# Optimization experiments

Measured on AMD Instinct MI355X. Metric: run time of the kernel, lower is better.

## Reference

```python
import math
import jax, jax.numpy as jnp
import numpy as np

B, LA, LB, H = 16, 1024, 1024, 512
NEG = -10000000.0


def setup_inputs() -> dict:
    key = jax.random.key(0)
    k1, k2, k3, k4 = jax.random.split(key, 4)
    a = jax.random.normal(k1, (B, LA, H), dtype=jnp.float32)
    b = jax.random.normal(k2, (B, LB, H), dtype=jnp.float32)
    mask_a = jax.random.randint(k3, (B, LA, 1), 0, 2, dtype=jnp.int32)
    mask_b = jax.random.randint(k4, (B, LB, 1), 0, 2, dtype=jnp.int32)
    temperature = jnp.asarray(1.0 / math.sqrt(H), dtype=jnp.float32)
    return {"a": a, "b": b, "mask_a": mask_a, "mask_b": mask_b, "temperature": temperature}


def reference(a, b, mask_a, mask_b, temperature):
    # attn[b,i,j] = <a_i, b_j> * temperature  -> [B, LA, LB]
    attn = jnp.einsum("bid,bjd->bij", a, b) * temperature
    # pairwise validity mask: outer product of per-token masks
    mask = jnp.einsum("bik,bjk->bij", mask_a.astype(jnp.float32), mask_b.astype(jnp.float32)) > 0
    attn = jnp.where(mask, attn, NEG)
    attn_a = jax.nn.softmax(attn, axis=1)  # softmax over a-tokens
    attn_b = jax.nn.softmax(attn, axis=2)  # softmax over b-tokens
    feature_b = jnp.einsum("bij,bid->bjd", attn_a, a)  # [B, LB, H]
    feature_a = jnp.einsum("bij,bjd->bid", attn_b, b)  # [B, LA, H]
    return (feature_a, feature_b)
```

## Files before the change

### kernel.cpp

```cpp
#include <hip/hip_runtime.h>
#include <hip/hip_bf16.h>

#define NB_ 16
#define LA_ 1024
#define LB_ 1024
#define H_  512

typedef __attribute__((ext_vector_type(8))) short short8;
typedef __attribute__((ext_vector_type(4))) float f32x4;

using bf16 = __hip_bfloat16;

__device__ __forceinline__ float bf2f(unsigned short u) {
    union { unsigned int i; float f; } c; c.i = ((unsigned)u) << 16; return c.f;
}
__device__ __forceinline__ unsigned short f2bf(float f) {
    bf16 h = __float2bfloat16(f);
    return *(unsigned short*)&h;
}

__device__ __forceinline__ void load_lds16(const void* g, void* l) {
    __builtin_amdgcn_global_load_lds(
        (const __attribute__((address_space(1))) void*)g,
        (__attribute__((address_space(3))) void*)l, 16, 0, 0);
}

template<int DB, int MODE>
__device__ __forceinline__ void gemm_tile_cnt(
    const unsigned short* __restrict__ gA, const unsigned short* __restrict__ gB,
    int lda, int ldb, size_t ko,
    unsigned short* lds, char* lA, char* lB,
    const int* aoff, const int* boff, f32x4 acc[8][4])
{
    const char* bA = (const char*)lds + DB * 32768;
    const char* bB = (const char*)lds + 65536 + DB * 32768;
    const int nxt = (DB ^ 1) * 32768;
    short8 av[4][2];
#pragma unroll
    for (int p = 0; p < 4; ++p) {
        const int pm = p >> 1, pn = p & 1;
        if (pn == 0) {
#pragma unroll
            for (int f = 0; f < 4; f++)
#pragma unroll
                for (int kk = 0; kk < 2; kk++)
                    av[f][kk] = *(const short8*)(bA + (aoff[pm * 4 + f] ^ (kk << 6)));
        }
        short8 bv[2][2];
#pragma unroll
        for (int f = 0; f < 2; f++)
#pragma unroll
            for (int kk = 0; kk < 2; kk++)
                bv[f][kk] = *(const short8*)(bB + (boff[pn * 2 + f] ^ (kk << 6)));
        if (MODE == 0) {
            if (p == 0) {
                load_lds16(gB + ko,                       lB + nxt);
                load_lds16(gB + ko + (size_t)64 * ldb,    lB + nxt + 8192);
            } else if (p == 1) {
                load_lds16(gB + ko + (size_t)128 * ldb,   lB + nxt + 16384);
                load_lds16(gB + ko + (size_t)192 * ldb,   lB + nxt + 24576);
            } else if (p == 2) {
                load_lds16(gA + ko,                       lA + nxt);
                load_lds16(gA + ko + (size_t)128 * lda,   lA + nxt + 16384);
            } else {
                load_lds16(gA + ko + (size_t)64 * lda,    lA + nxt + 8192);
                load_lds16(gA + ko + (size_t)192 * lda,   lA + nxt + 24576);
            }
        }
        __builtin_amdgcn_s_barrier();
        __builtin_amdgcn_s_setprio(1);
#pragma unroll
        for (int kk = 0; kk < 2; kk++)
#pragma unroll
            for (int f = 0; f < 2; f++)
#pragma unroll
                for (int m = 0; m < 4; m++)
                    acc[pm * 4 + m][pn * 2 + f] =
                        __builtin_amdgcn_mfma_f32_16x16x32_bf16(
                            av[m][kk], bv[f][kk],
                            acc[pm * 4 + m][pn * 2 + f], 0, 0, 0);
        __builtin_amdgcn_s_setprio(0);
        if (p == 1) {
            if (MODE == 0) asm volatile("s_waitcnt vmcnt(4)" ::: "memory");
            else           asm volatile("s_waitcnt vmcnt(0)" ::: "memory");
        }
        if (p == 3 && MODE == 0) asm volatile("s_waitcnt vmcnt(2)" ::: "memory");
        if (p < 3 || MODE == 0) __builtin_amdgcn_s_barrier();
    }
}

template<int DB, int MODE>
__device__ __forceinline__ void gemm_tile_drn(
    const unsigned short* __restrict__ gA, const unsigned short* __restrict__ gB,
    int lda, int ldb, size_t ko,
    unsigned short* lds, char* lA, char* lB,
    const int* aoff, const int* boff, f32x4 acc[8][4])
{
    const char* bA = (const char*)lds + DB * 32768;
    const char* bB = (const char*)lds + 65536 + DB * 32768;
    const int nxt = (DB ^ 1) * 32768;
    if (MODE == 0) {
#pragma unroll
        for (int s = 0; s < 4; s++) {
            load_lds16(gA + ko + (size_t)(s * 64) * lda, lA + nxt + s * 8192);
            load_lds16(gB + ko + (size_t)(s * 64) * ldb, lB + nxt + s * 8192);
        }
    }
    short8 av[4][2];
#pragma unroll
    for (int p = 0; p < 4; ++p) {
        const int pm = p >> 1, pn = p & 1;
        if (pn == 0) {
#pragma unroll
            for (int f = 0; f < 4; f++)
#pragma unroll
                for (int kk = 0; kk < 2; kk++)
                    av[f][kk] = *(const short8*)(bA + (aoff[pm * 4 + f] ^ (kk << 6)));
        }
        short8 bv[2][2];
#pragma unroll
        for (int f = 0; f < 2; f++)
#pragma unroll
            for (int kk = 0; kk < 2; kk++)
                bv[f][kk] = *(const short8*)(bB + (boff[pn * 2 + f] ^ (kk << 6)));
        __builtin_amdgcn_s_barrier();
        __builtin_amdgcn_s_setprio(1);
#pragma unroll
        for (int kk = 0; kk < 2; kk++)
#pragma unroll
            for (int f = 0; f < 2; f++)
#pragma unroll
                for (int m = 0; m < 4; m++)
                    acc[pm * 4 + m][pn * 2 + f] =
                        __builtin_amdgcn_mfma_f32_16x16x32_bf16(
                            av[m][kk], bv[f][kk],
                            acc[pm * 4 + m][pn * 2 + f], 0, 0, 0);
        __builtin_amdgcn_s_setprio(0);
        if (p < 3) __builtin_amdgcn_s_barrier();
    }
    __syncthreads();
}

template<int SCHED>
__device__ __forceinline__ void gemm_core256(
    const unsigned short* __restrict__ A, const unsigned short* __restrict__ B,
    int lda, int ldb, int K,
    unsigned short* lds, f32x4 acc[8][4])
{
    const int t = threadIdx.x;
    const int w = t >> 6, lane = t & 63;
    const int wr = w >> 2, wc = w & 3;
    const int lm = lane & 15, q = lane >> 4;

    int aoff[8], boff[4];
#pragma unroll
    for (int f = 0; f < 8; f++) {
        const int ra = wr * 128 + f * 16 + lm;
        aoff[f] = ra * 128 + ((q ^ (ra & 7)) << 4);
    }
#pragma unroll
    for (int f = 0; f < 4; f++) {
        const int rb = wc * 64 + f * 16 + lm;
        boff[f] = rb * 128 + ((q ^ (rb & 7)) << 4);
    }

    const int rstep = w * 8 + (lane >> 3);
    const int sc = (lane & 7) ^ (lane >> 3);
    const unsigned short* gA = A + (size_t)rstep * lda + sc * 8;
    const unsigned short* gB = B + (size_t)rstep * ldb + sc * 8;
    char* lA = (char*)lds + w * 1024;
    char* lB = (char*)lds + 65536 + w * 1024;
    const int NT = K >> 6;

    if (SCHED == 0) {
        load_lds16(gB,                       lB);
        load_lds16(gB + (size_t)64 * ldb,    lB + 8192);
        load_lds16(gB + (size_t)128 * ldb,   lB + 16384);
        load_lds16(gB + (size_t)192 * ldb,   lB + 24576);
        load_lds16(gA,                       lA);
        load_lds16(gA + (size_t)128 * lda,   lA + 16384);
        load_lds16(gA + (size_t)64 * lda,    lA + 8192);
        load_lds16(gA + (size_t)192 * lda,   lA + 24576);
        asm volatile("s_waitcnt vmcnt(2)" ::: "memory");
        __builtin_amdgcn_s_barrier();
        int kt = 0;
        for (; kt + 2 < NT; kt += 2) {
            gemm_tile_cnt<0, 0>(gA, gB, lda, ldb, (size_t)(kt + 1) * 64,
                                lds, lA, lB, aoff, boff, acc);
            gemm_tile_cnt<1, 0>(gA, gB, lda, ldb, (size_t)(kt + 2) * 64,
                                lds, lA, lB, aoff, boff, acc);
        }
        gemm_tile_cnt<0, 0>(gA, gB, lda, ldb, (size_t)(NT - 1) * 64,
                            lds, lA, lB, aoff, boff, acc);
        gemm_tile_cnt<1, 1>(gA, gB, lda, ldb, 0, lds, lA, lB, aoff, boff, acc);
    } else {
#pragma unroll
        for (int s = 0; s < 4; s++) {
            load_lds16(gA + (size_t)(s * 64) * lda, lA + s * 8192);
            load_lds16(gB + (size_t)(s * 64) * ldb, lB + s * 8192);
        }
        __syncthreads();
        int kt = 0;
        for (; kt + 2 < NT; kt += 2) {
            gemm_tile_drn<0, 0>(gA, gB, lda, ldb, (size_t)(kt + 1) * 64,
                                lds, lA, lB, aoff, boff, acc);
            gemm_tile_drn<1, 0>(gA, gB, lda, ldb, (size_t)(kt + 2) * 64,
                                lds, lA, lB, aoff, boff, acc);
        }
        gemm_tile_drn<0, 0>(gA, gB, lda, ldb, (size_t)(NT - 1) * 64,
                            lds, lA, lB, aoff, boff, acc);
        gemm_tile_drn<1, 1>(gA, gB, lda, ldb, 0, lds, lA, lB, aoff, boff, acc);
    }
    __syncthreads();
}

__global__ __launch_bounds__(512, 2) void k_gemm_attn(
    const unsigned short* __restrict__ a_bf, const unsigned short* __restrict__ b_bf,
    const int* __restrict__ mask_a, const int* __restrict__ mask_b,
    const float* __restrict__ temp_p,
    unsigned short* __restrict__ E, unsigned short* __restrict__ ET,
    float* __restrict__ l_row, float* __restrict__ l_col)
{
    __shared__ unsigned short lds[65536];

    const int g = blockIdx.x;
    const int batch = g & 15;
    const int qq = g >> 4;
    const int i0 = (qq >> 2) * 256, j0 = (qq & 3) * 256;

    const unsigned short* A = a_bf + (size_t)batch * LA_ * H_ + (size_t)i0 * H_;
    const unsigned short* B = b_bf + (size_t)batch * LB_ * H_ + (size_t)j0 * H_;
    f32x4 acc[8][4];
#pragma unroll
    for (int x = 0; x < 8; x++)
#pragma unroll
        for (int y = 0; y < 4; y++) acc[x][y] = 0;

    gemm_core256<1>(A, B, H_, H_, H_, lds, acc);

    const float temp = temp_p[0];
    const int t = threadIdx.x, w = t >> 6, lane = t & 63;
    const int wr = w >> 2, wc = w & 3, lm = lane & 15, q = lane >> 4;
    const int* map = mask_a + batch * LA_;
    const int* mbp = mask_b + batch * LB_;
    unsigned short* Ep  = E  + (size_t)batch * LA_ * LB_;
    unsigned short* ETp = ET + (size_t)batch * LB_ * LA_;
    float* lrp = l_row + batch * LA_;
    float* lcp = l_col + batch * LB_;

    int mb4[4];
#pragma unroll
    for (int fn = 0; fn < 4; fn++) mb4[fn] = mbp[j0 + wc * 64 + fn * 16 + lm];

#pragma unroll
    for (int fm = 0; fm < 8; fm++) {
        const int ilb = wr * 128 + fm * 16 + q * 4;
        int ma[4];
#pragma unroll
        for (int r = 0; r < 4; r++) ma[r] = map[i0 + ilb + r];
#pragma unroll
        for (int fn = 0; fn < 4; fn++) {
            const int jl = wc * 64 + fn * 16 + lm;
            ushort4 pk;
            unsigned short* pp = (unsigned short*)&pk;
#pragma unroll
            for (int r = 0; r < 4; r++) {
                const float e = (ma[r] && mb4[fn]) ? __expf(acc[fm][fn][r] * temp) : 0.0f;
                acc[fm][fn][r] = e;
                pp[r] = f2bf(e);
                const int il = ilb + r;
                lds[il * 256 + ((((jl >> 3) ^ ((il >> 1) & 15)) << 3) | (jl & 7))] = pp[r];
            }
            *(ushort4*)(ETp + (size_t)(j0 + jl) * LA_ + i0 + ilb) = pk;
        }
    }

#pragma unroll
    for (int fm = 0; fm < 8; fm++)
#pragma unroll
        for (int r = 0; r < 4; r++) {
            float s = acc[fm][0][r] + acc[fm][1][r] + acc[fm][2][r] + acc[fm][3][r];
            s += __shfl_xor(s, 1, 16); s += __shfl_xor(s, 2, 16);
            s += __shfl_xor(s, 4, 16); s += __shfl_xor(s, 8, 16);
            if (lm == 0) atomicAdd(&lrp[i0 + wr * 128 + fm * 16 + q * 4 + r], s);
        }
#pragma unroll
    for (int fn = 0; fn < 4; fn++) {
        float s = 0.0f;
#pragma unroll
        for (int fm = 0; fm < 8; fm++)
#pragma unroll
            for (int r = 0; r < 4; r++) s += acc[fm][fn][r];
        s += __shfl_xor(s, 16, 64); s += __shfl_xor(s, 32, 64);
        if (lane < 16) atomicAdd(&lcp[j0 + wc * 64 + fn * 16 + lm], s);
    }

    __syncthreads();
#pragma unroll
    for (int rep = 0; rep < 16; rep++) {
        const int il = (t >> 5) + rep * 16;
        const int c = t & 31;
        const int phys = c ^ ((il >> 1) & 15);
        short8 v = *(const short8*)(lds + il * 256 + phys * 8);
        *(short8*)(Ep + (size_t)(i0 + il) * LB_ + j0 + c * 8) = v;
    }
}

__global__ __launch_bounds__(512, 2) void k_gemm_feat(
    const unsigned short* __restrict__ E, const unsigned short* __restrict__ ET,
    const unsigned short* __restrict__ aT, const unsigned short* __restrict__ bT,
    const int* __restrict__ mask_a, const int* __restrict__ mask_b,
    const int* __restrict__ nA, const int* __restrict__ nB,
    const float* __restrict__ l_row, const float* __restrict__ l_col,
    const float* __restrict__ mean_a, const float* __restrict__ mean_b,
    float* __restrict__ out)
{
    __shared__ unsigned short lds[65536];

    const int g = blockIdx.x;
    const int zc = g & 31;
    const int qq = g >> 5;
    const int n0 = (qq & 1) * 256, m0 = (qq >> 1) * 256;

    const int batch = zc & 15;
    const bool isA = zc < 16;
    const unsigned short* Amat = (isA ? E : ET) + (size_t)batch * 1024 * 1024;
    const unsigned short* Bm   = (isA ? bT : aT) + (size_t)batch * H_ * 1024;
    const int* mp   = (isA ? mask_a : mask_b) + batch * 1024;
    const int nn    = (isA ? nB : nA)[batch];
    const float* sp = (isA ? l_row : l_col) + batch * 1024;
    const float* mv = (isA ? mean_b : mean_a) + batch * H_;
    float* op = out + (isA ? (size_t)0 : (size_t)NB_ * LA_ * H_) + (size_t)batch * 1024 * H_;

    f32x4 acc[8][4];
#pragma unroll
    for (int x = 0; x < 8; x++)
#pragma unroll
        for (int y = 0; y < 4; y++) acc[x][y] = 0;

    gemm_core256<0>(Amat + (size_t)m0 * 1024, Bm + (size_t)n0 * 1024,
                    1024, 1024, 1024, lds, acc);

    const int t = threadIdx.x, w = t >> 6, lane = t & 63;
    const int wr = w >> 2, wc = w & 3, lm = lane & 15, q = lane >> 4;

    float mval[4];
#pragma unroll
    for (int fn = 0; fn < 4; fn++) mval[fn] = mv[n0 + wc * 64 + fn * 16 + lm];

#pragma unroll
    for (int fm = 0; fm < 8; fm++) {
        const int ib = m0 + wr * 128 + fm * 16 + q * 4;
#pragma unroll
        for (int r = 0; r < 4; r++) {
            const int i = ib + r;
            const bool valid = (mp[i] != 0) && (nn > 0);
            const float inv = valid ? 1.0f / sp[i] : 0.0f;
#pragma unroll
            for (int fn = 0; fn < 4; fn++) {
                const int d = n0 + wc * 64 + fn * 16 + lm;
                op[(size_t)i * H_ + d] = valid ? acc[fm][fn][r] * inv : mval[fn];
            }
        }
    }
}

__global__ __launch_bounds__(256) void k_prep(
    const float* __restrict__ a, const float* __restrict__ b,
    unsigned short* __restrict__ aN, unsigned short* __restrict__ bN,
    unsigned short* __restrict__ aT, unsigned short* __restrict__ bT,
    float* __restrict__ mean_a, float* __restrict__ mean_b,
    const int* __restrict__ mask_a, const int* __restrict__ mask_b,
    int* __restrict__ nA, int* __restrict__ nB,
    float* __restrict__ zero_base)
{
    const int g = blockIdx.x, t = threadIdx.x;
    if (g >= 256) {
        const int s = g - 256;
        *(float4*)(zero_base + ((size_t)s * 256 + t) * 4) = make_float4(0, 0, 0, 0);
        const int batch = s & 15, which = s >> 4;
        const int* m = (which ? mask_b : mask_a) + batch * 1024;
        int cnt = m[t] + m[t + 256] + m[t + 512] + m[t + 768];
        __shared__ int red[256];
        red[t] = cnt;
        __syncthreads();
        for (int off = 128; off; off >>= 1) {
            if (t < off) red[t] += red[t + off];
            __syncthreads();
        }
        if (t == 0) (which ? nB : nA)[batch] = red[0];
        return;
    }
    const int dstrip = g & 7, batch = (g >> 3) & 15, sel = g >> 7;
    const float* src = (sel ? b : a) + (size_t)batch * 1024 * H_;
    unsigned short* np = (sel ? bN : aN) + (size_t)batch * 1024 * H_;
    unsigned short* tp = (sel ? bT : aT) + (size_t)batch * H_ * 1024;
    float* mdst = (sel ? mean_b : mean_a) + batch * H_;
    const int d0 = dstrip * 64;

    __shared__ unsigned short lds[64][68];
    __shared__ float cs[4][64];
    const int c4 = (t & 15) * 4;
    float colsum[4] = {0.f, 0.f, 0.f, 0.f};
    for (int i0 = 0; i0 < 1024; i0 += 64) {
#pragma unroll
        for (int it = 0; it < 4; it++) {
            const int r = (t >> 4) + it * 16;
            float4 v = *(const float4*)(src + (size_t)(i0 + r) * H_ + d0 + c4);
            colsum[0] += v.x; colsum[1] += v.y; colsum[2] += v.z; colsum[3] += v.w;
            ushort4 u = make_ushort4(f2bf(v.x), f2bf(v.y), f2bf(v.z), f2bf(v.w));
            *(ushort4*)(np + (size_t)(i0 + r) * H_ + d0 + c4) = u;
            *(ushort4*)&lds[r][c4] = u;
        }
        __syncthreads();
#pragma unroll
        for (int it = 0; it < 4; it++) {
            const int dd = (t >> 4) + it * 16;
            const int i4 = (t & 15) * 4;
            ushort4 u = make_ushort4(lds[i4][dd], lds[i4 + 1][dd],
                                     lds[i4 + 2][dd], lds[i4 + 3][dd]);
            *(ushort4*)(tp + (size_t)(d0 + dd) * 1024 + i0 + i4) = u;
        }
        __syncthreads();
    }
#pragma unroll
    for (int j = 0; j < 4; j++) {
        colsum[j] += __shfl_xor(colsum[j], 16, 64);
        colsum[j] += __shfl_xor(colsum[j], 32, 64);
    }
    const int w = t >> 6, lane = t & 63;
    if (lane < 16) {
#pragma unroll
        for (int j = 0; j < 4; j++) cs[w][c4 + j] = colsum[j];
    }
    __syncthreads();
    if (t < 64) mdst[d0 + t] = (cs[0][t] + cs[1][t] + cs[2][t] + cs[3][t]) * (1.0f / 1024.0f);
}

extern "C" void kernel_launch(void* const* d_in, const int* in_sizes, int n_in,
                              void* d_out, int out_size, void* d_ws, size_t ws_size,
                              hipStream_t stream)
{
    const float* a      = (const float*)d_in[0];
    const float* b      = (const float*)d_in[1];
    const int*   mask_a = (const int*)d_in[2];
    const int*   mask_b = (const int*)d_in[3];
    const float* temp   = (const float*)d_in[4];
    float* out = (float*)d_out;

    char* ws = (char*)d_ws;
    size_t off = 0;
    unsigned short* E    = (unsigned short*)(ws + off); off += (size_t)NB_ * LA_ * LB_ * 2;
    unsigned short* ET   = (unsigned short*)(ws + off); off += (size_t)NB_ * LB_ * LA_ * 2;
    unsigned short* a_bf = (unsigned short*)(ws + off); off += (size_t)NB_ * LA_ * H_ * 2;
    unsigned short* b_bf = (unsigned short*)(ws + off); off += (size_t)NB_ * LB_ * H_ * 2;
    unsigned short* aT   = (unsigned short*)(ws + off); off += (size_t)NB_ * H_ * LA_ * 2;
    unsigned short* bT   = (unsigned short*)(ws + off); off += (size_t)NB_ * H_ * LB_ * 2;
    float* l_row  = (float*)(ws + off); off += (size_t)NB_ * LA_ * 4;
    float* l_col  = (float*)(ws + off); off += (size_t)NB_ * LB_ * 4;
    float* mean_a = (float*)(ws + off); off += (size_t)NB_ * H_ * 4;
    float* mean_b = (float*)(ws + off); off += (size_t)NB_ * H_ * 4;
    int*   nA     = (int*)(ws + off); off += 64;
    int*   nB     = (int*)(ws + off); off += 64;

    k_prep<<<dim3(288), 256, 0, stream>>>(
        a, b, a_bf, b_bf, aT, bT, mean_a, mean_b,
        mask_a, mask_b, nA, nB, l_row);

    k_gemm_attn<<<dim3(256), 512, 0, stream>>>(
        a_bf, b_bf, mask_a, mask_b, temp, E, ET, l_row, l_col);

    k_gemm_feat<<<dim3(256), 512, 0, stream>>>(
        E, ET, aT, bT, mask_a, mask_b, nA, nB, l_row, l_col, mean_a, mean_b, out);
}
```

Baseline: 203.1 us.

## Fuse prep and both GEMM kernels into one cooperative kernel with grid syncs

Merges the prep, attention-GEMM and feature-GEMM kernels into a single cooperative launch of 256 blocks of 512 threads, separated by grid-wide barriers. The prep stage is re-tiled to 512 threads per block, and the mask-count and l_row zeroing are folded into a subset of blocks. The aim is to remove the inter-kernel launch gaps and tail drain between the three stages. In exchange it adds grid.sync overhead and requires all 256 blocks to be co-resident, and the prep stage now runs on fewer, larger blocks than before (256 blocks of 512 threads instead of 288 blocks of 256).

```diff
diff --git a/kernel.cpp b/kernel.cpp
--- a/kernel.cpp
+++ b/kernel.cpp
@@ -1,5 +1,8 @@
 #include <hip/hip_runtime.h>
 #include <hip/hip_bf16.h>
+#include <hip/hip_cooperative_groups.h>
+
+namespace cg = cooperative_groups;
 
 #define NB_ 16
 #define LA_ 1024
@@ -214,227 +217,229 @@
     __syncthreads();
 }
 
-__global__ __launch_bounds__(512, 2) void k_gemm_attn(
-    const unsigned short* __restrict__ a_bf, const unsigned short* __restrict__ b_bf,
+__global__ __launch_bounds__(512, 2) void k_fused(
+    const float* __restrict__ a, const float* __restrict__ b,
     const int* __restrict__ mask_a, const int* __restrict__ mask_b,
     const float* __restrict__ temp_p,
+    unsigned short* __restrict__ a_bf, unsigned short* __restrict__ b_bf,
+    unsigned short* __restrict__ aT, unsigned short* __restrict__ bT,
     unsigned short* __restrict__ E, unsigned short* __restrict__ ET,
-    float* __restrict__ l_row, float* __restrict__ l_col)
-{
-    __shared__ unsigned short lds[65536];
-
-    const int g = blockIdx.x;
-    const int batch = g & 15;
-    const int qq = g >> 4;
-    const int i0 = (qq >> 2) * 256, j0 = (qq & 3) * 256;
-
-    const unsigned short* A = a_bf + (size_t)batch * LA_ * H_ + (size_t)i0 * H_;
-    const unsigned short* B = b_bf + (size_t)batch * LB_ * H_ + (size_t)j0 * H_;
-    f32x4 acc[8][4];
-#pragma unroll
-    for (int x = 0; x < 8; x++)
-#pragma unroll
-        for (int y = 0; y < 4; y++) acc[x][y] = 0;
-
-    gemm_core256<1>(A, B, H_, H_, H_, lds, acc);
-
-    const float temp = temp_p[0];
-    const int t = threadIdx.x, w = t >> 6, lane = t & 63;
-    const int wr = w >> 2, wc = w & 3, lm = lane & 15, q = lane >> 4;
-    const int* map = mask_a + batch * LA_;
-    const int* mbp = mask_b + batch * LB_;
-    unsigned short* Ep  = E  + (size_t)batch * LA_ * LB_;
-    unsigned short* ETp = ET + (size_t)batch * LB_ * LA_;
-    float* lrp = l_row + batch * LA_;
-    float* lcp = l_col + batch * LB_;
-
-    int mb4[4];
-#pragma unroll
-    for (int fn = 0; fn < 4; fn++) mb4[fn] = mbp[j0 + wc * 64 + fn * 16 + lm];
-
-#pragma unroll
-    for (int fm = 0; fm < 8; fm++) {
-        const int ilb = wr * 128 + fm * 16 + q * 4;
-        int ma[4];
-#pragma unroll
-        for (int r = 0; r < 4; r++) ma[r] = map[i0 + ilb + r];
-#pragma unroll
-        for (int fn = 0; fn < 4; fn++) {
-            const int jl = wc * 64 + fn * 16 + lm;
-            ushort4 pk;
-            unsigned short* pp = (unsigned short*)&pk;
-#pragma unroll
-            for (int r = 0; r < 4; r++) {
-                const float e = (ma[r] && mb4[fn]) ? __expf(acc[fm][fn][r] * temp) : 0.0f;
-                acc[fm][fn][r] = e;
-                pp[r] = f2bf(e);
-                const int il = ilb + r;
-                lds[il * 256 + ((((jl >> 3) ^ ((il >> 1) & 15)) << 3) | (jl & 7))] = pp[r];
-            }
-            *(ushort4*)(ETp + (size_t)(j0 + jl) * LA_ + i0 + ilb) = pk;
-        }
-    }
-
-#pragma unroll
-    for (int fm = 0; fm < 8; fm++)
-#pragma unroll
-        for (int r = 0; r < 4; r++) {
-            float s = acc[fm][0][r] + acc[fm][1][r] + acc[fm][2][r] + acc[fm][3][r];
-            s += __shfl_xor(s, 1, 16); s += __shfl_xor(s, 2, 16);
-            s += __shfl_xor(s, 4, 16); s += __shfl_xor(s, 8, 16);
-            if (lm == 0) atomicAdd(&lrp[i0 + wr * 128 + fm * 16 + q * 4 + r], s);
-        }
-#pragma unroll
-    for (int fn = 0; fn < 4; fn++) {
-        float s = 0.0f;
-#pragma unroll
-        for (int fm = 0; fm < 8; fm++)
-#pragma unroll
-            for (int r = 0; r < 4; r++) s += acc[fm][fn][r];
-        s += __shfl_xor(s, 16, 64); s += __shfl_xor(s, 32, 64);
-        if (lane < 16) atomicAdd(&lcp[j0 + wc * 64 + fn * 16 + lm], s);
-    }
-
-    __syncthreads();
-#pragma unroll
-    for (int rep = 0; rep < 16; rep++) {
-        const int il = (t >> 5) + rep * 16;
-        const int c = t & 31;
-        const int phys = c ^ ((il >> 1) & 15);
-        short8 v = *(const short8*)(lds + il * 256 + phys * 8);
-        *(short8*)(Ep + (size_t)(i0 + il) * LB_ + j0 + c * 8) = v;
-    }
-}
-
-__global__ __launch_bounds__(512, 2) void k_gemm_feat(
-    const unsigned short* __restrict__ E, const unsigned short* __restrict__ ET,
-    const unsigned short* __restrict__ aT, const unsigned short* __restrict__ bT,
-    const int* __restrict__ mask_a, const int* __restrict__ mask_b,
-    const int* __restrict__ nA, const int* __restrict__ nB,
-    const float* __restrict__ l_row, const float* __restrict__ l_col,
-    const float* __restrict__ mean_a, const float* __restrict__ mean_b,
+    float* __restrict__ l_row, float* __restrict__ l_col,
+    float* __restrict__ mean_a, float* __restrict__ mean_b,
+    int* __restrict__ nA, int* __restrict__ nB,
     float* __restrict__ out)
 {
     __shared__ unsigned short lds[65536];
-
+    cg::grid_group grid = cg::this_grid();
     const int g = blockIdx.x;
-    const int zc = g & 31;
-    const int qq = g >> 5;
-    const int n0 = (qq & 1) * 256, m0 = (qq >> 1) * 256;
-
-    const int batch = zc & 15;
-    const bool isA = zc < 16;
-    const unsigned short* Amat = (isA ? E : ET) + (size_t)batch * 1024 * 1024;
-    const unsigned short* Bm   = (isA ? bT : aT) + (size_t)batch * H_ * 1024;
-    const int* mp   = (isA ? mask_a : mask_b) + batch * 1024;
-    const int nn    = (isA ? nB : nA)[batch];
-    const float* sp = (isA ? l_row : l_col) + batch * 1024;
-    const float* mv = (isA ? mean_b : mean_a) + batch * H_;
-    float* op = out + (isA ? (size_t)0 : (size_t)NB_ * LA_ * H_) + (size_t)batch * 1024 * H_;
-
-    f32x4 acc[8][4];
-#pragma unroll
-    for (int x = 0; x < 8; x++)
-#pragma unroll
-        for (int y = 0; y < 4; y++) acc[x][y] = 0;
-
-    gemm_core256<0>(Amat + (size_t)m0 * 1024, Bm + (size_t)n0 * 1024,
-                    1024, 1024, 1024, lds, acc);
-
-    const int t = threadIdx.x, w = t >> 6, lane = t & 63;
-    const int wr = w >> 2, wc = w & 3, lm = lane & 15, q = lane >> 4;
-
-    float mval[4];
-#pragma unroll
-    for (int fn = 0; fn < 4; fn++) mval[fn] = mv[n0 + wc * 64 + fn * 16 + lm];
-
-#pragma unroll
-    for (int fm = 0; fm < 8; fm++) {
-        const int ib = m0 + wr * 128 + fm * 16 + q * 4;
-#pragma unroll
-        for (int r = 0; r < 4; r++) {
-            const int i = ib + r;
-            const bool valid = (mp[i] != 0) && (nn > 0);
-            const float inv = valid ? 1.0f / sp[i] : 0.0f;
+    const int t = threadIdx.x;
+
+    {
+        const int dstrip = g & 7, batch = (g >> 3) & 15, sel = g >> 7;
+        const float* src = (sel ? b : a) + (size_t)batch * 1024 * H_;
+        unsigned short* np = (sel ? b_bf : a_bf) + (size_t)batch * 1024 * H_;
+        unsigned short* tp = (sel ? bT : aT) + (size_t)batch * H_ * 1024;
+        float* mdst = (sel ? mean_b : mean_a) + batch * H_;
+        const int d0 = dstrip * 64;
+        unsigned short (*tile)[68] = (unsigned short (*)[68])lds;
+        float* csf = (float*)((char*)lds + 32768);
+        int*   ired = (int*)((char*)lds + 36864);
+
+        const int c4 = (t & 15) * 4;
+        float colsum[4] = {0.f, 0.f, 0.f, 0.f};
+        for (int i0 = 0; i0 < 1024; i0 += 128) {
+#pragma unroll
+            for (int it = 0; it < 4; it++) {
+                const int r = (t >> 4) + it * 32;
+                float4 v = *(const float4*)(src + (size_t)(i0 + r) * H_ + d0 + c4);
+                colsum[0] += v.x; colsum[1] += v.y; colsum[2] += v.z; colsum[3] += v.w;
+                ushort4 u = make_ushort4(f2bf(v.x), f2bf(v.y), f2bf(v.z), f2bf(v.w));
+                *(ushort4*)(np + (size_t)(i0 + r) * H_ + d0 + c4) = u;
+                *(ushort4*)&tile[r][c4] = u;
+            }
+            __syncthreads();
+#pragma unroll
+            for (int it = 0; it < 4; it++) {
+                const int dd = (t >> 5) + it * 16;
+                const int i4 = (t & 31) * 4;
+                ushort4 u = make_ushort4(tile[i4][dd], tile[i4 + 1][dd],
+                                         tile[i4 + 2][dd], tile[i4 + 3][dd]);
+                *(ushort4*)(tp + (size_t)(d0 + dd) * 1024 + i0 + i4) = u;
+            }
+            __syncthreads();
+        }
+#pragma unroll
+        for (int j = 0; j < 4; j++) {
+            colsum[j] += __shfl_xor(colsum[j], 16, 64);
+            colsum[j] += __shfl_xor(colsum[j], 32, 64);
+        }
+        const int w = t >> 6, lane = t & 63;
+        if (lane < 16) {
+#pragma unroll
+            for (int j = 0; j < 4; j++) csf[w * 64 + c4 + j] = colsum[j];
+        }
+        __syncthreads();
+        if (t < 64) {
+            float s = 0.f;
+#pragma unroll
+            for (int w2 = 0; w2 < 8; w2++) s += csf[w2 * 64 + t];
+            mdst[d0 + t] = s * (1.0f / 1024.0f);
+        }
+        if (g < 16) {
+            *(float4*)(l_row + ((size_t)g * 512 + t) * 4) = make_float4(0, 0, 0, 0);
+        } else if (g < 48) {
+            const int s2 = g - 16, batch2 = s2 & 15, which = s2 >> 4;
+            const int* m = (which ? mask_b : mask_a) + batch2 * 1024;
+            int cnt = m[t] + m[t + 512];
+#pragma unroll
+            for (int off = 1; off < 64; off <<= 1) cnt += __shfl_xor(cnt, off, 64);
+            if (lane == 0) ired[w] = cnt;
+            __syncthreads();
+            if (t == 0) {
+                int s3 = 0;
+#pragma unroll
+                for (int w2 = 0; w2 < 8; w2++) s3 += ired[w2];
+                (which ? nB : nA)[batch2] = s3;
+            }
+        }
+    }
+    __threadfence();
+    grid.sync();
+    __threadfence();
+
+    {
+        const int batch = g & 15;
+        const int qq = g >> 4;
+        const int i0 = (qq >> 2) * 256, j0 = (qq & 3) * 256;
+
+        const unsigned short* A = a_bf + (size_t)batch * LA_ * H_ + (size_t)i0 * H_;
+        const unsigned short* B = b_bf + (size_t)batch * LB_ * H_ + (size_t)j0 * H_;
+        f32x4 acc[8][4];
+#pragma unroll
+        for (int x = 0; x < 8; x++)
+#pragma unroll
+            for (int y = 0; y < 4; y++) acc[x][y] = 0;
+
+        gemm_core256<1>(A, B, H_, H_, H_, lds, acc);
+
+        const float temp = temp_p[0];
+        const int w = t >> 6, lane = t & 63;
+        const int wr = w >> 2, wc = w & 3, lm = lane & 15, q = lane >> 4;
+        const int* map = mask_a + batch * LA_;
+        const int* mbp = mask_b + batch * LB_;
+        unsigned short* Ep  = E  + (size_t)batch * LA_ * LB_;
+        unsigned short* ETp = ET + (size_t)batch * LB_ * LA_;
+        float* lrp = l_row + batch * LA_;
+        float* lcp = l_col + batch * LB_;
+
+        int mb4[4];
+#pragma unroll
+        for (int fn = 0; fn < 4; fn++) mb4[fn] = mbp[j0 + wc * 64 + fn * 16 + lm];
+
+#pragma unroll
+        for (int fm = 0; fm < 8; fm++) {
+            const int ilb = wr * 128 + fm * 16 + q * 4;
+            int ma[4];
+#pragma unroll
+            for (int r = 0; r < 4; r++) ma[r] = map[i0 + ilb + r];
 #pragma unroll
             for (int fn = 0; fn < 4; fn++) {
-                const int d = n0 + wc * 64 + fn * 16 + lm;
-                op[(size_t)i * H_ + d] = valid ? acc[fm][fn][r] * inv : mval[fn];
-            }
-        }
-    }
-}
-
-__global__ __launch_bounds__(256) void k_prep(
-    const float* __restrict__ a, const float* __restrict__ b,
-    unsigned short* __restrict__ aN, unsigned short* __restrict__ bN,
-    unsigned short* __restrict__ aT, unsigned short* __restrict__ bT,
-    float* __restrict__ mean_a, float* __restrict__ mean_b,
-    const int* __restrict__ mask_a, const int* __restrict__ mask_b,
-    int* __restrict__ nA, int* __restrict__ nB,
-    float* __restrict__ zero_base)
-{
-    const int g = blockIdx.x, t = threadIdx.x;
-    if (g >= 256) {
-        const int s = g - 256;
-        *(float4*)(zero_base + ((size_t)s * 256 + t) * 4) = make_float4(0, 0, 0, 0);
-        const int batch = s & 15, which = s >> 4;
-        const int* m = (which ? mask_b : mask_a) + batch * 1024;
-        int cnt = m[t] + m[t + 256] + m[t + 512] + m[t + 768];
-        __shared__ int red[256];
-        red[t] = cnt;
+                const int jl = wc * 64 + fn * 16 + lm;
+                ushort4 pk;
+                unsigned short* pp = (unsigned short*)&pk;
+#pragma unroll
+                for (int r = 0; r < 4; r++) {
+                    const float e = (ma[r] && mb4[fn]) ? __expf(acc[fm][fn][r] * temp) : 0.0f;
+                    acc[fm][fn][r] = e;
+                    pp[r] = f2bf(e);
+                    const int il = ilb + r;
+                    lds[il * 256 + ((((jl >> 3) ^ ((il >> 1) & 15)) << 3) | (jl & 7))] = pp[r];
+                }
+                *(ushort4*)(ETp + (size_t)(j0 + jl) * LA_ + i0 + ilb) = pk;
+            }
+        }
+
+#pragma unroll
+        for (int fm = 0; fm < 8; fm++)
+#pragma unroll
+            for (int r = 0; r < 4; r++) {
+                float s = acc[fm][0][r] + acc[fm][1][r] + acc[fm][2][r] + acc[fm][3][r];
+                s += __shfl_xor(s, 1, 16); s += __shfl_xor(s, 2, 16);
+                s += __shfl_xor(s, 4, 16); s += __shfl_xor(s, 8, 16);
+                if (lm == 0) atomicAdd(&lrp[i0 + wr * 128 + fm * 16 + q * 4 + r], s);
+            }
+#pragma unroll
+        for (int fn = 0; fn < 4; fn++) {
+            float s = 0.0f;
+#pragma unroll
+            for (int fm = 0; fm < 8; fm++)
+#pragma unroll
+                for (int r = 0; r < 4; r++) s += acc[fm][fn][r];
+            s += __shfl_xor(s, 16, 64); s += __shfl_xor(s, 32, 64);
+            if (lane < 16) atomicAdd(&lcp[j0 + wc * 64 + fn * 16 + lm], s);
+        }
+
         __syncthreads();
-        for (int off = 128; off; off >>= 1) {
-            if (t < off) red[t] += red[t + off];
-            __syncthreads();
-        }
-        if (t == 0) (which ? nB : nA)[batch] = red[0];
-        return;
-    }
-    const int dstrip = g & 7, batch = (g >> 3) & 15, sel = g >> 7;
-    const float* src = (sel ? b : a) + (size_t)batch * 1024 * H_;
-    unsigned short* np = (sel ? bN : aN) + (size_t)batch * 1024 * H_;
-    unsigned short* tp = (sel ? bT : aT) + (size_t)batch * H_ * 1024;
-    float* mdst = (sel ? mean_b : mean_a) + batch * H_;
-    const int d0 = dstrip * 64;
-
-    __shared__ unsigned short lds[64][68];
-    __shared__ float cs[4][64];
-    const int c4 = (t & 15) * 4;
-    float colsum[4] = {0.f, 0.f, 0.f, 0.f};
-    for (int i0 = 0; i0 < 1024; i0 += 64) {
-#pragma unroll
-        for (int it = 0; it < 4; it++) {
-            const int r = (t >> 4) + it * 16;
-            float4 v = *(const float4*)(src + (size_t)(i0 + r) * H_ + d0 + c4);
-            colsum[0] += v.x; colsum[1] += v.y; colsum[2] += v.z; colsum[3] += v.w;
-            ushort4 u = make_ushort4(f2bf(v.x), f2bf(v.y), f2bf(v.z), f2bf(v.w));
-            *(ushort4*)(np + (size_t)(i0 + r) * H_ + d0 + c4) = u;
-            *(ushort4*)&lds[r][c4] = u;
-        }
-        __syncthreads();
-#pragma unroll
-        for (int it = 0; it < 4; it++) {
-            const int dd = (t >> 4) + it * 16;
-            const int i4 = (t & 15) * 4;
-            ushort4 u = make_ushort4(lds[i4][dd], lds[i4 + 1][dd],
-                                     lds[i4 + 2][dd], lds[i4 + 3][dd]);
-            *(ushort4*)(tp + (size_t)(d0 + dd) * 1024 + i0 + i4) = u;
-        }
-        __syncthreads();
-    }
-#pragma unroll
-    for (int j = 0; j < 4; j++) {
-        colsum[j] += __shfl_xor(colsum[j], 16, 64);
-        colsum[j] += __shfl_xor(colsum[j], 32, 64);
-    }
-    const int w = t >> 6, lane = t & 63;
-    if (lane < 16) {
-#pragma unroll
-        for (int j = 0; j < 4; j++) cs[w][c4 + j] = colsum[j];
-    }
-    __syncthreads();
-    if (t < 64) mdst[d0 + t] = (cs[0][t] + cs[1][t] + cs[2][t] + cs[3][t]) * (1.0f / 1024.0f);
+#pragma unroll
+        for (int rep = 0; rep < 16; rep++) {
+            const int il = (t >> 5) + rep * 16;
+            const int c = t & 31;
+            const int phys = c ^ ((il >> 1) & 15);
+            short8 v = *(const short8*)(lds + il * 256 + phys * 8);
+            *(short8*)(Ep + (size_t)(i0 + il) * LB_ + j0 + c * 8) = v;
+        }
+    }
+    __threadfence();
+    grid.sync();
+    __threadfence();
+
+    {
+        const int zc = g & 31;
+        const int qq = g >> 5;
+        const int n0 = (qq & 1) * 256, m0 = (qq >> 1) * 256;
+
+        const int batch = zc & 15;
+        const bool isA = zc < 16;
+        const unsigned short* Amat = (isA ? E : ET) + (size_t)batch * 1024 * 1024;
+        const unsigned short* Bm   = (isA ? bT : aT) + (size_t)batch * H_ * 1024;
+        const int* mp   = (isA ? mask_a : mask_b) + batch * 1024;
+        const int nn    = (isA ? nB : nA)[batch];
+        const float* sp = (isA ? l_row : l_col) + batch * 1024;
+        const float* mv = (isA ? mean_b : mean_a) + batch * H_;
+        float* op = out + (isA ? (size_t)0 : (size_t)NB_ * LA_ * H_) + (size_t)batch * 1024 * H_;
+
+        f32x4 acc[8][4];
+#pragma unroll
+        for (int x = 0; x < 8; x++)
+#pragma unroll
+            for (int y = 0; y < 4; y++) acc[x][y] = 0;
+
+        gemm_core256<0>(Amat + (size_t)m0 * 1024, Bm + (size_t)n0 * 1024,
+                        1024, 1024, 1024, lds, acc);
+
+        const int w = t >> 6, lane = t & 63;
+        const int wr = w >> 2, wc = w & 3, lm = lane & 15, q = lane >> 4;
+
+        float mval[4];
+#pragma unroll
+        for (int fn = 0; fn < 4; fn++) mval[fn] = mv[n0 + wc * 64 + fn * 16 + lm];
+
+#pragma unroll
+        for (int fm = 0; fm < 8; fm++) {
+            const int ib = m0 + wr * 128 + fm * 16 + q * 4;
+#pragma unroll
+            for (int r = 0; r < 4; r++) {
+                const int i = ib + r;
+                const bool valid = (mp[i] != 0) && (nn > 0);
+                const float inv = valid ? 1.0f / sp[i] : 0.0f;
+#pragma unroll
+                for (int fn = 0; fn < 4; fn++) {
+                    const int d = n0 + wc * 64 + fn * 16 + lm;
+                    op[(size_t)i * H_ + d] = valid ? acc[fm][fn][r] * inv : mval[fn];
+                }
+            }
+        }
+    }
 }
 
 extern "C" void kernel_launch(void* const* d_in, const int* in_sizes, int n_in,
@@ -463,13 +468,12 @@
     int*   nA     = (int*)(ws + off); off += 64;
     int*   nB     = (int*)(ws + off); off += 64;
 
-    k_prep<<<dim3(288), 256, 0, stream>>>(
-        a, b, a_bf, b_bf, aT, bT, mean_a, mean_b,
-        mask_a, mask_b, nA, nB, l_row);
-
-    k_gemm_attn<<<dim3(256), 512, 0, stream>>>(
-        a_bf, b_bf, mask_a, mask_b, temp, E, ET, l_row, l_col);
-
-    k_gemm_feat<<<dim3(256), 512, 0, stream>>>(
-        E, ET, aT, bT, mask_a, mask_b, nA, nB, l_row, l_col, mean_a, mean_b, out);
-}
+    void* args[] = {
+        (void*)&a, (void*)&b, (void*)&mask_a, (void*)&mask_b, (void*)&temp,
+        (void*)&a_bf, (void*)&b_bf, (void*)&aT, (void*)&bT,
+        (void*)&E, (void*)&ET, (void*)&l_row, (void*)&l_col,
+        (void*)&mean_a, (void*)&mean_b, (void*)&nA, (void*)&nB, (void*)&out
+    };
+    hipLaunchCooperativeKernel((const void*)k_fused, dim3(256), dim3(512),
+                               args, 0, stream);
+}
```

Result: slower. 456.3 us (+124.7%).
